# Optimization experiments

Hardware: AMD Instinct MI355X
Metric: run time of the kernel (lower is better)

The kernel has to match this reference:

```python
import jax, jax.numpy as jnp
import numpy as np

# config matching init_kwargs
C = 256; G = 16; GC = C // G; K = 3; P = K * K
PAD = 1; STR = 1; DIL = 1; OFFSET_SCALE = 1.0
N, H, W = 8, 64, 64


def setup_inputs() -> dict:
    key = jax.random.key(0)
    ks = jax.random.split(key, 8)
    def rn(k, shape, sc):
        return jax.random.normal(k, shape, jnp.float32) * sc
    return {
        "x": jax.random.normal(ks[0], (N, H, W, C), jnp.float32),
        "dw_w": rn(ks[1], (C, 1, K, K), 0.1),          # depthwise conv weight (OIHW, groups=C)
        "dw_b": jnp.zeros((C,), jnp.float32),
        "ln_g": jnp.ones((C,), jnp.float32),
        "ln_b": jnp.zeros((C,), jnp.float32),
        "off_w": rn(ks[2], (G * P * 2, C), 0.01),      # offset head (small so offsets stay sane)
        "off_b": jnp.zeros((G * P * 2,), jnp.float32),
        "mask_w": rn(ks[3], (G * P, C), 0.01),
        "mask_b": jnp.zeros((G * P,), jnp.float32),
        "in_w": rn(ks[4], (C, C), 0.05),
        "in_b": jnp.zeros((C,), jnp.float32),
        "out_w": rn(ks[5], (C, C), 0.05),
        "out_b": jnp.zeros((C,), jnp.float32),
    }


def _layer_norm(x, g, b, eps=1e-6):
    m = x.mean(-1, keepdims=True)
    v = ((x - m) ** 2).mean(-1, keepdims=True)
    return (x - m) * jax.lax.rsqrt(v + eps) * g + b


def _grid_sample_bilinear(img, grid):
    # img: (B, Cc, Hh, Ww); grid: (B, L, P, 2) normalized to [-1, 1], (x, y) order.
    # Matches torch.grid_sample(mode='bilinear', padding_mode='zeros', align_corners=False).
    B, Cc, Hh, Ww = img.shape
    gx = (grid[..., 0] + 1.0) * (Ww * 0.5) - 0.5
    gy = (grid[..., 1] + 1.0) * (Hh * 0.5) - 0.5
    x0 = jnp.floor(gx); y0 = jnp.floor(gy)
    tx = gx - x0; ty = gy - y0
    img_f = img.reshape(B, Cc, Hh * Ww)
    def corner(xi, yi, w):
        valid = (xi >= 0) & (xi < Ww) & (yi >= 0) & (yi < Hh)
        idx = (jnp.clip(yi, 0, Hh - 1) * Ww + jnp.clip(xi, 0, Ww - 1)).astype(jnp.int32)
        v = jnp.take_along_axis(img_f, idx.reshape(B, 1, -1), axis=2)  # (B, Cc, L*P)
        return v * (w * valid).reshape(B, 1, -1)
    out = (corner(x0, y0, (1 - tx) * (1 - ty)) + corner(x0 + 1, y0, tx * (1 - ty))
           + corner(x0, y0 + 1, (1 - tx) * ty) + corner(x0 + 1, y0 + 1, tx * ty))
    return out.reshape(B, Cc, grid.shape[1], grid.shape[2])  # (B, Cc, L, P)


def _dcnv3_core(x, offset, mask):
    # x: (N,H,W,C) value features; offset: (N,H,W,G*P*2); mask: (N,H,W,G*P)
    xpad = jnp.pad(x, ((0, 0), (PAD, PAD), (PAD, PAD), (0, 0)))
    Hi, Wi = H + 2 * PAD, W + 2 * PAD
    Ho, Wo = H, W
    # reference points (centers of receptive field), normalized by padded size
    start = (DIL * (K - 1)) // 2 + 0.5
    ry = (start + jnp.arange(Ho, dtype=jnp.float32) * STR) / Hi
    rx = (start + jnp.arange(Wo, dtype=jnp.float32) * STR) / Wi
    ref = jnp.stack([jnp.broadcast_to(rx[None, :], (Ho, Wo)),
                     jnp.broadcast_to(ry[:, None], (Ho, Wo))], -1)  # (Ho,Wo,2) (x,y)
    # dilation grid, x-major flattening to match torch meshgrid('ij') ordering
    d = jnp.arange(K, dtype=jnp.float32) * DIL - (DIL * (K - 1)) // 2
    kgrid = jnp.stack([jnp.repeat(d, K) / Wi, jnp.tile(d, K) / Hi], -1)  # (P,2)
    off = offset.reshape(N, Ho, Wo, G, P, 2)
    norm = jnp.array([Wi, Hi], jnp.float32)
    loc = (ref[None, :, :, None, None, :]
           + kgrid[None, None, None, None, :, :] * OFFSET_SCALE
           + off * OFFSET_SCALE / norm)                      # (N,Ho,Wo,G,P,2)
    sg = (2.0 * loc - 1.0).reshape(N, Ho * Wo, G, P, 2)
    sg = sg.transpose(0, 2, 1, 3, 4).reshape(N * G, Ho * Wo, P, 2)
    val = xpad.reshape(N, Hi * Wi, G * GC).transpose(0, 2, 1).reshape(N * G, GC, Hi, Wi)
    samp = _grid_sample_bilinear(val, sg)                    # (N*G, GC, Ho*Wo, P)
    m = mask.reshape(N, Ho * Wo, G, P).transpose(0, 2, 1, 3).reshape(N * G, 1, Ho * Wo, P)
    out = (samp * m).sum(-1)                                 # (N*G, GC, Ho*Wo)
    return out.reshape(N, G * GC, Ho * Wo).transpose(0, 2, 1).reshape(N, Ho, Wo, C)


def reference(x, dw_w, dw_b, ln_g, ln_b, off_w, off_b, mask_w, mask_b, in_w, in_b, out_w, out_b):
    xp = x @ in_w.T + in_b                                   # input_proj (values)
    # depthwise conv -> LN (channels_last) -> exact GELU
    y = jax.lax.conv_general_dilated(
        x.transpose(0, 3, 1, 2), dw_w, (1, 1), ((PAD, PAD), (PAD, PAD)),
        feature_group_count=C, dimension_numbers=('NCHW', 'OIHW', 'NCHW'))
    y = y + dw_b[None, :, None, None]
    x1 = jax.nn.gelu(_layer_norm(y.transpose(0, 2, 3, 1), ln_g, ln_b), approximate=False)
    offset = x1 @ off_w.T + off_b                            # (N,H,W,G*P*2)
    mlogits = (x1 @ mask_w.T + mask_b).reshape(N, H, W, G, P)
    mask = jax.nn.softmax(mlogits, axis=-1).reshape(N, H, W, G * P)
    out = _dcnv3_core(xp, offset, mask)
    return out @ out_w.T + out_b
```

## Files before the change

### kernel.cpp

```cpp
#include <hip/hip_runtime.h>


#define LL 32768
#define CC 256

typedef __bf16 bf16;
typedef __bf16 bf16x4 __attribute__((ext_vector_type(4)));
typedef __bf16 bf16x8 __attribute__((ext_vector_type(8)));
typedef float f32x4v __attribute__((ext_vector_type(4)));

__device__ __forceinline__ void gload16(const bf16* g, const bf16* lds_base) {
    __builtin_amdgcn_global_load_lds(
        (const __attribute__((address_space(1))) void*)g,
        (__attribute__((address_space(3))) void*)lds_base, 16, 0, 0);
}

__global__ __launch_bounds__(256) void k_prep(
    const float* __restrict__ in_w, const float* __restrict__ off_w,
    const float* __restrict__ mask_w, const float* __restrict__ out_w,
    const float* __restrict__ dw_w, const float* __restrict__ off_b,
    const float* __restrict__ mask_b,
    bf16* __restrict__ in_h, bf16* __restrict__ hw_h,
    bf16* __restrict__ out_h,
    float* __restrict__ dwT, float* __restrict__ hbias) {
    int idx = blockIdx.x * 256 + threadIdx.x;
    if (idx < 60416) {
        const float* s; bf16* hi; int i;
        if (idx < 16384)      { s = in_w;   hi = in_h;          i = idx; }
        else if (idx < 34816) { s = off_w;  hi = hw_h;          i = idx - 16384; }
        else if (idx < 44032) { s = mask_w; hi = hw_h + 73728;  i = idx - 34816; }
        else                  { s = out_w;  hi = out_h;         i = idx - 44032; }
        float4 v = *(const float4*)(s + (size_t)i * 4);
        bf16x4 h;
        h[0] = (bf16)v.x; h[1] = (bf16)v.y; h[2] = (bf16)v.z; h[3] = (bf16)v.w;
        *(bf16x4*)(hi + (size_t)i * 4) = h;
    } else if (idx < 62720) {
        int e = idx - 60416;
        int c = e & 255, j = e >> 8;
        dwT[j * 256 + c] = dw_w[c * 9 + j];
    } else if (idx < 63232) {
        int e = idx - 62720;
        hbias[e] = (e < 288) ? off_b[e] : (e < 432 ? mask_b[e - 288] : 0.f);
    } else if (idx < 68352) {
        int e = idx - 63232;
        bf16x4 z = {(bf16)0.f, (bf16)0.f, (bf16)0.f, (bf16)0.f};
        *(bf16x4*)(hw_h + 110592 + (size_t)e * 4) = z;
    }
}

__global__ __launch_bounds__(256) void k_dwln(
    const float* __restrict__ x, const float* __restrict__ dwT,
    const float* __restrict__ dw_b, const float* __restrict__ ln_g,
    const float* __restrict__ ln_b, bf16* __restrict__ x1h,
    bf16* __restrict__ xb) {
    int t = threadIdx.x;
    int q = t >> 6, u = t & 63;
    int l = blockIdx.x * 4 + q;
    int w = l & 63, h = (l >> 6) & 63, n = l >> 12;
    int c0 = u * 4;

    float4 acc = *(const float4*)(dw_b + c0);
    float4 xc = {0.f, 0.f, 0.f, 0.f};
#pragma unroll
    for (int kh = 0; kh < 3; ++kh) {
        int hh = h + kh - 1;
        if (hh < 0 || hh >= 64) continue;
#pragma unroll
        for (int kw = 0; kw < 3; ++kw) {
            int ww = w + kw - 1;
            if (ww < 0 || ww >= 64) continue;
            float4 xv = *(const float4*)(x + (size_t)(((n * 64 + hh) * 64) + ww) * CC + c0);
            if (kh == 1 && kw == 1) xc = xv;
            float4 wv = *(const float4*)(dwT + (kh * 3 + kw) * 256 + c0);
            acc.x += xv.x * wv.x; acc.y += xv.y * wv.y;
            acc.z += xv.z * wv.z; acc.w += xv.w * wv.w;
        }
    }
    bf16x4 xcb;
    xcb[0] = (bf16)xc.x; xcb[1] = (bf16)xc.y;
    xcb[2] = (bf16)xc.z; xcb[3] = (bf16)xc.w;
    *(bf16x4*)(xb + (size_t)l * CC + c0) = xcb;

    float s = acc.x + acc.y + acc.z + acc.w;
    float ss = acc.x * acc.x + acc.y * acc.y + acc.z * acc.z + acc.w * acc.w;
#pragma unroll
    for (int d = 1; d < 64; d <<= 1) {
        s += __shfl_xor(s, d);
        ss += __shfl_xor(ss, d);
    }
    float mean = s * (1.0f / 256.0f);
    float var = ss * (1.0f / 256.0f) - mean * mean;
    float rstd = rsqrtf(var + 1e-6f);
    float4 gv = *(const float4*)(ln_g + c0);
    float4 bv = *(const float4*)(ln_b + c0);
    float xn0 = (acc.x - mean) * rstd * gv.x + bv.x;
    float xn1 = (acc.y - mean) * rstd * gv.y + bv.y;
    float xn2 = (acc.z - mean) * rstd * gv.z + bv.z;
    float xn3 = (acc.w - mean) * rstd * gv.w + bv.w;
    bf16x4 oh;
    oh[0] = (bf16)(0.5f * xn0 * (1.0f + erff(xn0 * 0.70710678118654752f)));
    oh[1] = (bf16)(0.5f * xn1 * (1.0f + erff(xn1 * 0.70710678118654752f)));
    oh[2] = (bf16)(0.5f * xn2 * (1.0f + erff(xn2 * 0.70710678118654752f)));
    oh[3] = (bf16)(0.5f * xn3 * (1.0f + erff(xn3 * 0.70710678118654752f)));
    *(bf16x4*)(x1h + (size_t)l * CC + c0) = oh;
}

template <bool OBF16>
__global__ __launch_bounds__(256) void k_gemm(
    const bf16* __restrict__ A, const bf16* __restrict__ Wh,
    const float* __restrict__ bias, float* __restrict__ C32,
    bf16* __restrict__ Cbf, int Nout) {
    int mb = blockIdx.x * 128, nb = blockIdx.y * 128;
    int t = threadIdx.x, wave = t >> 6, lane = t & 63;
    int wm = wave & 1, wn = wave >> 1;
    int fm = lane & 15, fq = lane >> 4;

    __shared__ bf16 smem[8192];

    const bf16* gbase[4];
    const bf16* lbase[4];
#pragma unroll
    for (int j = 0; j < 4; ++j) {
        int seg = wave * 4 + j;
        int arr = seg >> 3;
        int row = (seg & 7) * 16 + (lane >> 2);
        int col = (lane & 3) * 8;
        const bf16* g = (arr == 0) ? (A + (size_t)(mb + row) * CC + col)
                                   : (Wh + (size_t)(nb + row) * CC + col);
        gbase[j] = g;
        lbase[j] = smem + seg * 512;
    }

    f32x4v acc[4][4];
#pragma unroll
    for (int i = 0; i < 4; ++i)
#pragma unroll
        for (int j = 0; j < 4; ++j) acc[i][j] = (f32x4v){0.f, 0.f, 0.f, 0.f};

    for (int kc = 0; kc < 256; kc += 32) {
#pragma unroll
        for (int j = 0; j < 4; ++j) gload16(gbase[j] + kc, lbase[j]);
        __syncthreads();

        bf16x8 af[4], bfh[4];
#pragma unroll
        for (int i = 0; i < 4; ++i)
            af[i] = *(const bf16x8*)&smem[(wm * 64 + i * 16 + fm) * 32 + fq * 8];
#pragma unroll
        for (int j = 0; j < 4; ++j)
            bfh[j] = *(const bf16x8*)&smem[4096 + (wn * 64 + j * 16 + fm) * 32 + fq * 8];
#pragma unroll
        for (int i = 0; i < 4; ++i)
#pragma unroll
            for (int j = 0; j < 4; ++j)
                acc[i][j] = __builtin_amdgcn_mfma_f32_16x16x32_bf16(
                    af[i], bfh[j], acc[i][j], 0, 0, 0);
        __syncthreads();
    }

#pragma unroll
    for (int j = 0; j < 4; ++j) {
        int n_g = nb + wn * 64 + j * 16 + fm;
        if (n_g >= Nout) continue;
        float bv = bias[n_g];
#pragma unroll
        for (int i = 0; i < 4; ++i) {
            int m_g = mb + wm * 64 + i * 16 + fq * 4;
#pragma unroll
            for (int rg = 0; rg < 4; ++rg) {
                float o = acc[i][j][rg] + bv;
                if (OBF16)
                    Cbf[(size_t)(m_g + rg) * Nout + n_g] = (bf16)o;
                else
                    C32[(size_t)(m_g + rg) * Nout + n_g] = o;
            }
        }
    }
}

__global__ __launch_bounds__(256) void k_gather(
    const bf16* __restrict__ xp, const bf16* __restrict__ head,
    bf16* __restrict__ rows) {
    int t = threadIdx.x;
    int q = t >> 5, u = t & 31;
    int l = blockIdx.x * 8 + q;
    int w = l & 63, h = (l >> 6) & 63, n = l >> 12;

    __shared__ float offs[8][288];
    __shared__ float ms[8][144];
    for (int j = u; j < 288; j += 32) offs[q][j] = (float)head[(size_t)l * 432 + j];
    for (int j = u; j < 144; j += 32) ms[q][j] = (float)head[(size_t)l * 432 + 288 + j];
    __syncthreads();

    if (u < 16) {
        int g = u;
        float mx = -1e30f;
#pragma unroll
        for (int p = 0; p < 9; ++p) mx = fmaxf(mx, ms[q][g * 9 + p]);
        float s = 0.f, e[9];
#pragma unroll
        for (int p = 0; p < 9; ++p) { e[p] = expf(ms[q][g * 9 + p] - mx); s += e[p]; }
        float inv = 1.0f / s;
#pragma unroll
        for (int p = 0; p < 9; ++p) ms[q][g * 9 + p] = e[p] * inv;
    }
    __syncthreads();

    int g = u >> 1;
    int c0 = g * 16 + (u & 1) * 8;
    const bf16* base = xp + (size_t)n * 4096 * CC + c0;
    float a0 = 0.f, a1 = 0.f, a2 = 0.f, a3 = 0.f;
    float a4 = 0.f, a5 = 0.f, a6 = 0.f, a7 = 0.f;
#pragma unroll
    for (int p = 0; p < 9; ++p) {
        float ox = offs[q][g * 18 + p * 2 + 0];
        float oy = offs[q][g * 18 + p * 2 + 1];
        float ax = (float)(w + (p / 3) - 1) + ox;
        float ay = (float)(h + (p % 3) - 1) + oy;
        float x0f = floorf(ax), y0f = floorf(ay);
        int x0 = (int)x0f, y0 = (int)y0f;
        float tx = ax - x0f, ty = ay - y0f;
        float m = ms[q][g * 9 + p];
        int idx[4]; float cw[4];
#pragma unroll
        for (int cr = 0; cr < 4; ++cr) {
            int xx = x0 + (cr & 1), yy = y0 + (cr >> 1);
            bool v = (xx >= 0) & (xx < 64) & (yy >= 0) & (yy < 64);
            int xc = min(max(xx, 0), 63), yc = min(max(yy, 0), 63);
            idx[cr] = (yc * 64 + xc) * CC;
            float wx = (cr & 1) ? tx : (1.f - tx);
            float wy = (cr >> 1) ? ty : (1.f - ty);
            cw[cr] = v ? (m * wx * wy) : 0.f;
        }
#pragma unroll
        for (int cr = 0; cr < 4; ++cr) {
            bf16x8 vb = *(const bf16x8*)(base + idx[cr]);
            float wt = cw[cr];
            a0 += wt * (float)vb[0]; a1 += wt * (float)vb[1];
            a2 += wt * (float)vb[2]; a3 += wt * (float)vb[3];
            a4 += wt * (float)vb[4]; a5 += wt * (float)vb[5];
            a6 += wt * (float)vb[6]; a7 += wt * (float)vb[7];
        }
    }
    bf16x8 oh;
    oh[0] = (bf16)a0; oh[1] = (bf16)a1; oh[2] = (bf16)a2; oh[3] = (bf16)a3;
    oh[4] = (bf16)a4; oh[5] = (bf16)a5; oh[6] = (bf16)a6; oh[7] = (bf16)a7;
    *(bf16x8*)(rows + (size_t)l * CC + c0) = oh;
}

__device__ __forceinline__ float dot256f(const float* a, const float* wrow) {
    const float4* w4 = (const float4*)wrow;
    float s = 0.f;
#pragma unroll 16
    for (int i = 0; i < 64; ++i) {
        float4 u = w4[i];
        const float* ap = a + i * 4;
        s += ap[0] * u.x + ap[1] * u.y + ap[2] * u.z + ap[3] * u.w;
    }
    return s;
}

__global__ __launch_bounds__(256) void k_inproj_fb(
    const float* __restrict__ x, const float* __restrict__ in_w,
    const float* __restrict__ in_b, float* __restrict__ xp) {
    int l = blockIdx.x;
    int t = threadIdx.x;
    __shared__ float xa[256];
    xa[t] = x[l * CC + t];
    __syncthreads();
    xp[l * CC + t] = dot256f(xa, in_w + t * CC) + in_b[t];
}

__device__ __forceinline__ float fetch_px_fb(const float* base, int yy, int xx) {
    if (xx < 0 || xx >= 64 || yy < 0 || yy >= 64) return 0.f;
    return base[(yy * 64 + xx) * CC];
}

__global__ __launch_bounds__(256) void k_main_fb(
    const float* __restrict__ x, const float* __restrict__ xp,
    const float* __restrict__ dw_w, const float* __restrict__ dw_b,
    const float* __restrict__ ln_g, const float* __restrict__ ln_b,
    const float* __restrict__ off_w, const float* __restrict__ off_b,
    const float* __restrict__ mask_w, const float* __restrict__ mask_b,
    const float* __restrict__ out_w, const float* __restrict__ out_b,
    float* __restrict__ out) {
    int l = blockIdx.x;
    int t = threadIdx.x;
    int w = l & 63, h = (l >> 6) & 63, n = l >> 12;
    __shared__ float x1[256];
    __shared__ float red[256];
    __shared__ float offs[288];
    __shared__ float ms[144];
    __shared__ float row[256];

    float acc = dw_b[t];
#pragma unroll
    for (int kh = 0; kh < 3; ++kh) {
        int hh = h + kh - 1;
        if (hh < 0 || hh >= 64) continue;
#pragma unroll
        for (int kw = 0; kw < 3; ++kw) {
            int ww = w + kw - 1;
            if (ww < 0 || ww >= 64) continue;
            acc += x[(((n * 64 + hh) * 64) + ww) * CC + t] * dw_w[t * 9 + kh * 3 + kw];
        }
    }
    red[t] = acc;
    __syncthreads();
    for (int s = 128; s > 0; s >>= 1) {
        if (t < s) red[t] += red[t + s];
        __syncthreads();
    }
    float mean = red[0] * (1.0f / 256.0f);
    __syncthreads();
    float d = acc - mean;
    red[t] = d * d;
    __syncthreads();
    for (int s = 128; s > 0; s >>= 1) {
        if (t < s) red[t] += red[t + s];
        __syncthreads();
    }
    float var = red[0] * (1.0f / 256.0f);
    float xn = d * rsqrtf(var + 1e-6f) * ln_g[t] + ln_b[t];
    x1[t] = 0.5f * xn * (1.0f + erff(xn * 0.70710678118654752f));
    __syncthreads();

    offs[t] = dot256f(x1, off_w + t * CC) + off_b[t];
    if (t < 32) {
        int j = 256 + t;
        offs[j] = dot256f(x1, off_w + j * CC) + off_b[j];
    }
    if (t < 144) ms[t] = dot256f(x1, mask_w + t * CC) + mask_b[t];
    __syncthreads();

    if (t < 16) {
        int g = t;
        float mx = -1e30f;
#pragma unroll
        for (int p = 0; p < 9; ++p) mx = fmaxf(mx, ms[g * 9 + p]);
        float s = 0.f, e[9];
#pragma unroll
        for (int p = 0; p < 9; ++p) { e[p] = expf(ms[g * 9 + p] - mx); s += e[p]; }
        float inv = 1.0f / s;
#pragma unroll
        for (int p = 0; p < 9; ++p) ms[g * 9 + p] = e[p] * inv;
    }
    __syncthreads();

    int g = t >> 4;
    const float* base = xp + (size_t)n * 64 * 64 * CC + t;
    float acc2 = 0.f;
#pragma unroll
    for (int p = 0; p < 9; ++p) {
        float ox = offs[g * 18 + p * 2 + 0];
        float oy = offs[g * 18 + p * 2 + 1];
        float ax = (float)(w + (p / 3) - 1) + ox;
        float ay = (float)(h + (p % 3) - 1) + oy;
        float x0f = floorf(ax), y0f = floorf(ay);
        int x0 = (int)x0f, y0 = (int)y0f;
        float tx = ax - x0f, ty = ay - y0f;
        float v00 = fetch_px_fb(base, y0, x0);
        float v01 = fetch_px_fb(base, y0, x0 + 1);
        float v10 = fetch_px_fb(base, y0 + 1, x0);
        float v11 = fetch_px_fb(base, y0 + 1, x0 + 1);
        float bl = (v00 * (1.f - tx) + v01 * tx) * (1.f - ty) +
                   (v10 * (1.f - tx) + v11 * tx) * ty;
        acc2 += ms[g * 9 + p] * bl;
    }
    row[t] = acc2;
    __syncthreads();
    out[l * CC + t] = dot256f(row, out_w + t * CC) + out_b[t];
}

extern "C" void kernel_launch(void* const* d_in, const int* in_sizes, int n_in,
                              void* d_out, int out_size, void* d_ws,
                              size_t ws_size, hipStream_t stream) {
    const float* x      = (const float*)d_in[0];
    const float* dw_w   = (const float*)d_in[1];
    const float* dw_b   = (const float*)d_in[2];
    const float* ln_g   = (const float*)d_in[3];
    const float* ln_b   = (const float*)d_in[4];
    const float* off_w  = (const float*)d_in[5];
    const float* off_b  = (const float*)d_in[6];
    const float* mask_w = (const float*)d_in[7];
    const float* mask_b = (const float*)d_in[8];
    const float* in_w   = (const float*)d_in[9];
    const float* in_b   = (const float*)d_in[10];
    const float* out_w  = (const float*)d_in[11];
    const float* out_b  = (const float*)d_in[12];
    float* out = (float*)d_out;

    const size_t szBF    = (size_t)LL * CC * 2;
    const size_t szHEADB = (size_t)LL * 432 * 2;
    const size_t szWB    = 1048576;
    const size_t need    = 3 * szBF + szHEADB + szWB;

    dim3 blk(256);
    if (ws_size >= need) {
        char* p = (char*)d_ws;
        bf16* x1h = (bf16*)p; p += szBF;
        bf16* xpb = (bf16*)p; p += szBF;
        bf16* xb  = (bf16*)p; p += szBF;
        bf16* headb = (bf16*)p; p += szHEADB;
        bf16* in_h  = (bf16*)p; p += 131072;
        bf16* hw_h  = (bf16*)p; p += 262144;
        bf16* out_h = (bf16*)p; p += 131072;
        float* dwT  = (float*)p; p += 9216;
        float* hbias = (float*)p;
        bf16* rows = x1h;

        k_prep<<<dim3(267), blk, 0, stream>>>(in_w, off_w, mask_w, out_w, dw_w,
                                              off_b, mask_b, in_h, hw_h, out_h,
                                              dwT, hbias);
        k_dwln<<<dim3(LL / 4), blk, 0, stream>>>(x, dwT, dw_b, ln_g, ln_b, x1h, xb);
        k_gemm<true><<<dim3(256, 2), blk, 0, stream>>>(
            xb, in_h, in_b, nullptr, xpb, 256);
        k_gemm<true><<<dim3(256, 4), blk, 0, stream>>>(
            x1h, hw_h, hbias, nullptr, headb, 432);
        k_gather<<<dim3(LL / 8), blk, 0, stream>>>(xpb, headb, rows);
        k_gemm<false><<<dim3(256, 2), blk, 0, stream>>>(
            rows, out_h, out_b, out, nullptr, 256);
    } else {
        float* xp = (float*)d_ws;
        k_inproj_fb<<<dim3(LL), blk, 0, stream>>>(x, in_w, in_b, xp);
        k_main_fb<<<dim3(LL), blk, 0, stream>>>(x, xp, dw_w, dw_b, ln_g, ln_b,
                                                off_w, off_b, mask_w, mask_b,
                                                out_w, out_b, out);
    }
}
```

Before: 209.3 us.

## Precompute bilinear corner weights once per sample point and use packed bf16 MACs

```diff
diff --git a/kernel.cpp b/kernel.cpp
--- a/kernel.cpp
+++ b/kernel.cpp
@@ -8,6 +8,7 @@
 typedef __bf16 bf16x4 __attribute__((ext_vector_type(4)));
 typedef __bf16 bf16x8 __attribute__((ext_vector_type(8)));
 typedef float f32x4v __attribute__((ext_vector_type(4)));
+typedef float f32x2 __attribute__((ext_vector_type(2)));
 
 __device__ __forceinline__ void gload16(const bf16* g, const bf16* lds_base) {
     __builtin_amdgcn_global_load_lds(
@@ -178,6 +179,19 @@
     }
 }
 
+__device__ __forceinline__ void mac8(f32x2 acc[4], bf16x8 v, float wt) {
+    union { bf16x8 b; unsigned u[4]; } cu;
+    cu.b = v;
+    f32x2 wv = {wt, wt};
+#pragma unroll
+    for (int i = 0; i < 4; ++i) {
+        f32x2 a;
+        a.x = __uint_as_float(cu.u[i] << 16);
+        a.y = __uint_as_float(cu.u[i] & 0xffff0000u);
+        acc[i] += a * wv;
+    }
+}
+
 __global__ __launch_bounds__(256) void k_gather(
     const bf16* __restrict__ xp, const bf16* __restrict__ head,
     bf16* __restrict__ rows) {
@@ -186,65 +200,94 @@
     int l = blockIdx.x * 8 + q;
     int w = l & 63, h = (l >> 6) & 63, n = l >> 12;
 
-    __shared__ float offs[8][288];
-    __shared__ float ms[8][144];
-    for (int j = u; j < 288; j += 32) offs[q][j] = (float)head[(size_t)l * 432 + j];
-    for (int j = u; j < 144; j += 32) ms[q][j] = (float)head[(size_t)l * 432 + 288 + j];
+    __shared__ float CW[8][576];
+    __shared__ int BASE[8][144];
+
+    for (int j = u; j < 432; j += 32) CW[q][j] = (float)head[(size_t)l * 432 + j];
     __syncthreads();
 
     if (u < 16) {
         int g = u;
         float mx = -1e30f;
 #pragma unroll
-        for (int p = 0; p < 9; ++p) mx = fmaxf(mx, ms[q][g * 9 + p]);
+        for (int p = 0; p < 9; ++p) mx = fmaxf(mx, CW[q][288 + g * 9 + p]);
         float s = 0.f, e[9];
 #pragma unroll
-        for (int p = 0; p < 9; ++p) { e[p] = expf(ms[q][g * 9 + p] - mx); s += e[p]; }
+        for (int p = 0; p < 9; ++p) { e[p] = expf(CW[q][288 + g * 9 + p] - mx); s += e[p]; }
         float inv = 1.0f / s;
 #pragma unroll
-        for (int p = 0; p < 9; ++p) ms[q][g * 9 + p] = e[p] * inv;
+        for (int p = 0; p < 9; ++p) CW[q][288 + g * 9 + p] = e[p] * inv;
+    }
+    __syncthreads();
+
+    float4 cwr[5];
+    int baser[5];
+#pragma unroll
+    for (int k = 0; k < 5; ++k) {
+        if (k < 4 || u < 16) {
+            int ei = u + 32 * k;
+            int g = ei / 9, p = ei - g * 9;
+            float ox = CW[q][g * 18 + p * 2 + 0];
+            float oy = CW[q][g * 18 + p * 2 + 1];
+            float m  = CW[q][288 + ei];
+            float ax = (float)(w + (p / 3) - 1) + ox;
+            float ay = (float)(h + (p % 3) - 1) + oy;
+            float x0f = floorf(ax), y0f = floorf(ay);
+            int x0 = (int)x0f, y0 = (int)y0f;
+            float tx = ax - x0f, ty = ay - y0f;
+            int xb, yb;
+            float wxa, wxb, wya, wyb;
+            if (x0 < 0)       { xb = 0;  wxa = (x0 == -1) ? tx : 0.f; wxb = 0.f; }
+            else if (x0 > 62) { xb = 62; wxa = 0.f; wxb = (x0 == 63) ? (1.f - tx) : 0.f; }
+            else              { xb = x0; wxa = 1.f - tx; wxb = tx; }
+            if (y0 < 0)       { yb = 0;  wya = (y0 == -1) ? ty : 0.f; wyb = 0.f; }
+            else if (y0 > 62) { yb = 62; wya = 0.f; wyb = (y0 == 63) ? (1.f - ty) : 0.f; }
+            else              { yb = y0; wya = 1.f - ty; wyb = ty; }
+            float4 cw;
+            cw.x = m * wxa * wya; cw.y = m * wxb * wya;
+            cw.z = m * wxa * wyb; cw.w = m * wxb * wyb;
+            cwr[k] = cw;
+            baser[k] = (n << 20) + (yb * 64 + xb) * 256;
+        }
+    }
+    __syncthreads();
+#pragma unroll
+    for (int k = 0; k < 5; ++k) {
+        if (k < 4 || u < 16) {
+            int ei = u + 32 * k;
+            *(float4*)&CW[q][ei * 4] = cwr[k];
+            BASE[q][ei] = baser[k];
+        }
     }
     __syncthreads();
 
     int g = u >> 1;
     int c0 = g * 16 + (u & 1) * 8;
-    const bf16* base = xp + (size_t)n * 4096 * CC + c0;
-    float a0 = 0.f, a1 = 0.f, a2 = 0.f, a3 = 0.f;
-    float a4 = 0.f, a5 = 0.f, a6 = 0.f, a7 = 0.f;
+    const bf16* xpc = xp + c0;
+    f32x2 acc[4];
+    acc[0] = (f32x2){0.f, 0.f}; acc[1] = (f32x2){0.f, 0.f};
+    acc[2] = (f32x2){0.f, 0.f}; acc[3] = (f32x2){0.f, 0.f};
 #pragma unroll
     for (int p = 0; p < 9; ++p) {
-        float ox = offs[q][g * 18 + p * 2 + 0];
-        float oy = offs[q][g * 18 + p * 2 + 1];
-        float ax = (float)(w + (p / 3) - 1) + ox;
-        float ay = (float)(h + (p % 3) - 1) + oy;
-        float x0f = floorf(ax), y0f = floorf(ay);
-        int x0 = (int)x0f, y0 = (int)y0f;
-        float tx = ax - x0f, ty = ay - y0f;
-        float m = ms[q][g * 9 + p];
-        int idx[4]; float cw[4];
-#pragma unroll
-        for (int cr = 0; cr < 4; ++cr) {
-            int xx = x0 + (cr & 1), yy = y0 + (cr >> 1);
-            bool v = (xx >= 0) & (xx < 64) & (yy >= 0) & (yy < 64);
-            int xc = min(max(xx, 0), 63), yc = min(max(yy, 0), 63);
-            idx[cr] = (yc * 64 + xc) * CC;
-            float wx = (cr & 1) ? tx : (1.f - tx);
-            float wy = (cr >> 1) ? ty : (1.f - ty);
-            cw[cr] = v ? (m * wx * wy) : 0.f;
-        }
-#pragma unroll
-        for (int cr = 0; cr < 4; ++cr) {
-            bf16x8 vb = *(const bf16x8*)(base + idx[cr]);
-            float wt = cw[cr];
-            a0 += wt * (float)vb[0]; a1 += wt * (float)vb[1];
-            a2 += wt * (float)vb[2]; a3 += wt * (float)vb[3];
-            a4 += wt * (float)vb[4]; a5 += wt * (float)vb[5];
-            a6 += wt * (float)vb[6]; a7 += wt * (float)vb[7];
-        }
+        int ei = g * 9 + p;
+        float4 cw = *(const float4*)&CW[q][ei * 4];
+        int base = BASE[q][ei];
+        const bf16* p0 = xpc + base;
+        const bf16* p1 = p0 + 16384;
+        bf16x8 v00 = *(const bf16x8*)(p0);
+        bf16x8 v01 = *(const bf16x8*)(p0 + 256);
+        bf16x8 v10 = *(const bf16x8*)(p1);
+        bf16x8 v11 = *(const bf16x8*)(p1 + 256);
+        mac8(acc, v00, cw.x);
+        mac8(acc, v01, cw.y);
+        mac8(acc, v10, cw.z);
+        mac8(acc, v11, cw.w);
     }
     bf16x8 oh;
-    oh[0] = (bf16)a0; oh[1] = (bf16)a1; oh[2] = (bf16)a2; oh[3] = (bf16)a3;
-    oh[4] = (bf16)a4; oh[5] = (bf16)a5; oh[6] = (bf16)a6; oh[7] = (bf16)a7;
+    oh[0] = (bf16)acc[0].x; oh[1] = (bf16)acc[0].y;
+    oh[2] = (bf16)acc[1].x; oh[3] = (bf16)acc[1].y;
+    oh[4] = (bf16)acc[2].x; oh[5] = (bf16)acc[2].y;
+    oh[6] = (bf16)acc[3].x; oh[7] = (bf16)acc[3].y;
     *(bf16x8*)(rows + (size_t)l * CC + c0) = oh;
 }
 
```

Result: faster. 204.2 us (-2.4%).
